# Kernel tuning notes

Measured on AMD Instinct MI355X. Metric: run time of the kernel, lower is better.

## Reference

```python
import jax, jax.numpy as jnp
import numpy as np

NEG_SLOPE = 0.01  # nn.LeakyReLU default used in module

def leaky_relu(x):
    return jnp.where(x >= 0, x, NEG_SLOPE * x)

def setup_inputs() -> dict:
    key = jax.random.key(0)
    k1, k2, k3, k4, k5 = jax.random.split(key, 5)
    B, S, D, H, E = 4, 2048, 1024, 2048, 8
    s_in = 1.0 / np.sqrt(D)
    return {
        "inputs": jax.random.normal(k1, (B, S, D), dtype=jnp.float32),
        "Wg": jax.random.normal(k2, (E, D), dtype=jnp.float32) * s_in,
        "bg": jax.random.normal(k3, (E,), dtype=jnp.float32) * s_in,
        "We": jax.random.normal(k4, (E, H, D), dtype=jnp.float32) * s_in,
        "be": jax.random.normal(k5, (E, H), dtype=jnp.float32) * s_in,
    }

def reference(inputs, Wg, bg, We, be):
    # gate: [B,S,E]
    gate_logits = jnp.einsum('bsd,ed->bse', inputs, Wg) + bg
    gate_probs = jax.nn.softmax(gate_logits, axis=-1)
    # all experts densely: [B,S,E,H]
    expert_out = leaky_relu(jnp.einsum('bsd,ehd->bseh', inputs, We) + be)
    # gate-weighted reduction over experts: [B,S,H]
    weighted = jnp.einsum('bseh,bse->bsh', expert_out, gate_probs)
    return weighted
```

## Files before the change

### kernel.cpp

```cpp
#include <hip/hip_runtime.h>
#include <hip/hip_bf16.h>
#include <math.h>

#define M_TOK 8192
#define N_H   2048
#define K_D   1024
#define N_E   8

typedef __bf16 bf16x8 __attribute__((ext_vector_type(8)));
typedef __bf16 bf16x4 __attribute__((ext_vector_type(4)));
typedef float  f32x4  __attribute__((ext_vector_type(4)));

__device__ inline f32x4 mfma16(bf16x8 a, bf16x8 b, f32x4 c) {
  return __builtin_amdgcn_mfma_f32_16x16x32_bf16(a, b, c, 0, 0, 0);
}

__device__ inline void load16_lds(const void* g, void* l) {
  __builtin_amdgcn_global_load_lds(
      (const __attribute__((address_space(1))) void*)g,
      (__attribute__((address_space(3))) void*)l, 16, 0, 0);
}

__global__ __launch_bounds__(256) void cvt_kernel(const float* __restrict__ src,
                                                  __bf16* __restrict__ dst,
                                                  int n4) {
  int i = blockIdx.x * blockDim.x + threadIdx.x;
  const int stride = gridDim.x * blockDim.x;
  for (; i < n4; i += stride) {
    float4 v = ((const float4*)src)[i];
    bf16x4 o = {(__bf16)v.x, (__bf16)v.y, (__bf16)v.z, (__bf16)v.w};
    *(bf16x4*)(dst + (size_t)i * 4) = o;
  }
}

__global__ __launch_bounds__(256) void gate_kernel(const float* __restrict__ X,
                                                   const float* __restrict__ Wg,
                                                   const float* __restrict__ bg,
                                                   float* __restrict__ gate) {
  const int tid = threadIdx.x;
  const int lane = tid & 63;
  const int wv = tid >> 6;
  const int token = blockIdx.x * 4 + wv;
  const float* xrow = X + (size_t)token * K_D;

  float xr[16];
#pragma unroll
  for (int i = 0; i < 16; ++i) xr[i] = xrow[lane + i * 64];

  float l[N_E];
#pragma unroll
  for (int e = 0; e < N_E; ++e) {
    const float* wrow = Wg + e * K_D;
    float s = 0.f;
#pragma unroll
    for (int i = 0; i < 16; ++i) s += xr[i] * wrow[lane + i * 64];
#pragma unroll
    for (int off = 32; off > 0; off >>= 1) s += __shfl_xor(s, off);
    l[e] = s + bg[e];
  }
  float mx = l[0];
#pragma unroll
  for (int e = 1; e < N_E; ++e) mx = fmaxf(mx, l[e]);
  float p[N_E], den = 0.f;
#pragma unroll
  for (int e = 0; e < N_E; ++e) { p[e] = expf(l[e] - mx); den += p[e]; }
  const float inv = 1.f / den;
  if (lane == 0) {
#pragma unroll
    for (int e = 0; e < N_E; ++e) gate[(size_t)token * N_E + e] = p[e] * inv;
  }
}

__global__ __launch_bounds__(256, 2) void moe_main(
    const __bf16* __restrict__ Xb, const __bf16* __restrict__ Wb,
    const float* __restrict__ gate, const float* __restrict__ be,
    float* __restrict__ out) {
  __shared__ __bf16 As[128 * 32];
  __shared__ __bf16 Bs[256 * 32];
  __shared__ float gS[128 * 8];
  __shared__ float bS[8 * 128];

  const int tid = threadIdx.x;
  const int lane = tid & 63;
  const int wv = tid >> 6;
  const int wr = wv >> 1, wn = wv & 1;
  const int row0 = blockIdx.x * 128;
  const int col0 = blockIdx.y * 128;

  for (int i = tid; i < 1024; i += 256) {
    gS[i] = gate[(size_t)row0 * N_E + i];
    bS[i] = be[(size_t)(i >> 7) * N_H + col0 + (i & 127)];
  }

  const int rA = tid >> 2;
  const int kk = (tid & 3) * 8;
  const __bf16* aP0 = Xb + (size_t)(row0 + rA) * K_D + kk;
  const __bf16* aP1 = aP0 + (size_t)64 * K_D;

  const int lr = lane & 15;
  const int lk = (lane >> 4) * 8;
  const __bf16* aRd = &As[(wr * 64 + lr) * 32 + lk];
  const __bf16* bRd = &Bs[(wn * 64 + lr) * 32 + lk];

  f32x4 fin[4][4];
#pragma unroll
  for (int m = 0; m < 4; ++m)
#pragma unroll
    for (int h = 0; h < 4; ++h) fin[m][h] = (f32x4){0.f, 0.f, 0.f, 0.f};

  for (int p = 0; p < 4; ++p) {
    const int e0 = p * 2;

    const __bf16* bP0 = Wb + ((size_t)(e0 + 0) * N_H + col0 + 0  + rA) * K_D + kk;
    const __bf16* bP1 = Wb + ((size_t)(e0 + 0) * N_H + col0 + 64 + rA) * K_D + kk;
    const __bf16* bP2 = Wb + ((size_t)(e0 + 1) * N_H + col0 + 0  + rA) * K_D + kk;
    const __bf16* bP3 = Wb + ((size_t)(e0 + 1) * N_H + col0 + 64 + rA) * K_D + kk;

    f32x4 acc[4][8];
#pragma unroll
    for (int m = 0; m < 4; ++m)
#pragma unroll
      for (int n = 0; n < 8; ++n) acc[m][n] = (f32x4){0.f, 0.f, 0.f, 0.f};

    for (int kt = 0; kt < K_D / 32; ++kt) {
      const int k0 = kt * 32;
      __syncthreads();
      load16_lds(aP0 + k0, &As[wv * 512]);
      load16_lds(aP1 + k0, &As[2048 + wv * 512]);
      load16_lds(bP0 + k0, &Bs[wv * 512]);
      load16_lds(bP1 + k0, &Bs[2048 + wv * 512]);
      load16_lds(bP2 + k0, &Bs[4096 + wv * 512]);
      load16_lds(bP3 + k0, &Bs[6144 + wv * 512]);
      __syncthreads();

      bf16x8 af[4];
#pragma unroll
      for (int m = 0; m < 4; ++m) af[m] = *(const bf16x8*)(aRd + m * 16 * 32);
#pragma unroll
      for (int n = 0; n < 8; ++n) {
        const bf16x8 bfr =
            *(const bf16x8*)(bRd + ((n >> 2) * 128 + (n & 3) * 16) * 32);
#pragma unroll
        for (int m = 0; m < 4; ++m)
          acc[m][n] = mfma16(af[m], bfr, acc[m][n]);
      }
    }

#pragma unroll
    for (int m = 0; m < 4; ++m) {
#pragma unroll
      for (int j = 0; j < 4; ++j) {
        const int r = wr * 64 + m * 16 + (lane >> 4) * 4 + j;
        const float g0 = gS[r * 8 + e0];
        const float g1 = gS[r * 8 + e0 + 1];
#pragma unroll
        for (int h = 0; h < 4; ++h) {
          const int c = wn * 64 + h * 16 + lr;
          float v0 = acc[m][h][j] + bS[e0 * 128 + c];
          v0 = (v0 >= 0.f) ? v0 : 0.01f * v0;
          float v1 = acc[m][4 + h][j] + bS[(e0 + 1) * 128 + c];
          v1 = (v1 >= 0.f) ? v1 : 0.01f * v1;
          fin[m][h][j] += g0 * v0 + g1 * v1;
        }
      }
    }
  }

#pragma unroll
  for (int m = 0; m < 4; ++m) {
#pragma unroll
    for (int j = 0; j < 4; ++j) {
      const size_t r = (size_t)(row0 + wr * 64 + m * 16 + (lane >> 4) * 4 + j);
#pragma unroll
      for (int h = 0; h < 4; ++h) {
        out[r * N_H + col0 + wn * 64 + h * 16 + lr] = fin[m][h][j];
      }
    }
  }
}

extern "C" void kernel_launch(void* const* d_in, const int* in_sizes, int n_in,
                              void* d_out, int out_size, void* d_ws, size_t ws_size,
                              hipStream_t stream) {
  const float* X  = (const float*)d_in[0];
  const float* Wg = (const float*)d_in[1];
  const float* bg = (const float*)d_in[2];
  const float* We = (const float*)d_in[3];
  const float* be = (const float*)d_in[4];
  float* out = (float*)d_out;

  char* ws = (char*)d_ws;
  __bf16* Xb   = (__bf16*)(ws);
  __bf16* Wb   = (__bf16*)(ws + (size_t)16 * 1024 * 1024);
  float*  gate = (float*)(ws + (size_t)48 * 1024 * 1024);

  cvt_kernel<<<2048, 256, 0, stream>>>(X, Xb, (M_TOK * K_D) / 4);
  cvt_kernel<<<2048, 256, 0, stream>>>(We, Wb, (N_E * N_H * K_D) / 4);

  gate_kernel<<<M_TOK / 4, 256, 0, stream>>>(X, Wg, bg, gate);

  dim3 grid(M_TOK / 128, N_H / 128);
  moe_main<<<grid, 256, 0, stream>>>(Xb, Wb, gate, be, out);
}
```

Measured before the change: 331.9 us.

## Double-buffer LDS in MoE GEMM and fuse X conversion into gate kernel

The main GEMM loop now flattens the four expert-pair passes into one 128-step pipeline. Global-to-LDS loads for the next k-tile go into a second buffer while MFMAs run on the current one, which removes one barrier per step. The gate epilogue is applied every 32 steps, and s_setprio is raised around the MFMA block. The separate fp32-to-bf16 conversion of X is folded into the gate kernel, which already reads X, removing one kernel launch and one full pass over X. LDS use doubles, which may reduce occupancy, and the stores of Xb from the gate kernel are scalar 2-byte writes.

After: 314.2 us. -5.3%, faster.

```diff
diff --git a/kernel.cpp b/kernel.cpp
--- a/kernel.cpp
+++ b/kernel.cpp
@@ -36,7 +36,8 @@
 __global__ __launch_bounds__(256) void gate_kernel(const float* __restrict__ X,
                                                    const float* __restrict__ Wg,
                                                    const float* __restrict__ bg,
-                                                   float* __restrict__ gate) {
+                                                   float* __restrict__ gate,
+                                                   __bf16* __restrict__ Xb) {
   const int tid = threadIdx.x;
   const int lane = tid & 63;
   const int wv = tid >> 6;
@@ -47,6 +48,10 @@
 #pragma unroll
   for (int i = 0; i < 16; ++i) xr[i] = xrow[lane + i * 64];
 
+#pragma unroll
+  for (int i = 0; i < 16; ++i)
+    Xb[(size_t)token * K_D + lane + i * 64] = (__bf16)xr[i];
+
   float l[N_E];
 #pragma unroll
   for (int e = 0; e < N_E; ++e) {
@@ -75,8 +80,8 @@
     const __bf16* __restrict__ Xb, const __bf16* __restrict__ Wb,
     const float* __restrict__ gate, const float* __restrict__ be,
     float* __restrict__ out) {
-  __shared__ __bf16 As[128 * 32];
-  __shared__ __bf16 Bs[256 * 32];
+  __shared__ __bf16 As[2][128 * 32];
+  __shared__ __bf16 Bs[2][256 * 32];
   __shared__ float gS[128 * 8];
   __shared__ float bS[8 * 128];
 
@@ -94,13 +99,15 @@
 
   const int rA = tid >> 2;
   const int kk = (tid & 3) * 8;
-  const __bf16* aP0 = Xb + (size_t)(row0 + rA) * K_D + kk;
-  const __bf16* aP1 = aP0 + (size_t)64 * K_D;
+  const __bf16* aB = Xb + (size_t)(row0 + rA) * K_D + kk;
+  const __bf16* bB = Wb + (size_t)(col0 + rA) * K_D + kk;
 
   const int lr = lane & 15;
   const int lk = (lane >> 4) * 8;
-  const __bf16* aRd = &As[(wr * 64 + lr) * 32 + lk];
-  const __bf16* bRd = &Bs[(wn * 64 + lr) * 32 + lk];
+  const __bf16* aRd0 = &As[0][(wr * 64 + lr) * 32 + lk];
+  const __bf16* aRd1 = &As[1][(wr * 64 + lr) * 32 + lk];
+  const __bf16* bRd0 = &Bs[0][(wn * 64 + lr) * 32 + lk];
+  const __bf16* bRd1 = &Bs[1][(wn * 64 + lr) * 32 + lk];
 
   f32x4 fin[4][4];
 #pragma unroll
@@ -108,44 +115,27 @@
 #pragma unroll
     for (int h = 0; h < 4; ++h) fin[m][h] = (f32x4){0.f, 0.f, 0.f, 0.f};
 
-  for (int p = 0; p < 4; ++p) {
+  f32x4 acc[4][8];
+#pragma unroll
+  for (int m = 0; m < 4; ++m)
+#pragma unroll
+    for (int n = 0; n < 8; ++n) acc[m][n] = (f32x4){0.f, 0.f, 0.f, 0.f};
+
+  auto STAGE = [&](int tn, int bufN) {
+    const int k0 = (tn & 31) << 5;
+    const size_t pOff = (size_t)(tn >> 5) << 22;
+    const __bf16* a = aB + k0;
+    load16_lds(a, &As[bufN][wv * 512]);
+    load16_lds(a + (size_t)64 * K_D, &As[bufN][2048 + wv * 512]);
+    const __bf16* b = bB + pOff + k0;
+    load16_lds(b, &Bs[bufN][wv * 512]);
+    load16_lds(b + (size_t)64 * K_D, &Bs[bufN][2048 + wv * 512]);
+    load16_lds(b + (size_t)N_H * K_D, &Bs[bufN][4096 + wv * 512]);
+    load16_lds(b + (size_t)(N_H + 64) * K_D, &Bs[bufN][6144 + wv * 512]);
+  };
+
+  auto EPI = [&](int p) {
     const int e0 = p * 2;
-
-    const __bf16* bP0 = Wb + ((size_t)(e0 + 0) * N_H + col0 + 0  + rA) * K_D + kk;
-    const __bf16* bP1 = Wb + ((size_t)(e0 + 0) * N_H + col0 + 64 + rA) * K_D + kk;
-    const __bf16* bP2 = Wb + ((size_t)(e0 + 1) * N_H + col0 + 0  + rA) * K_D + kk;
-    const __bf16* bP3 = Wb + ((size_t)(e0 + 1) * N_H + col0 + 64 + rA) * K_D + kk;
-
-    f32x4 acc[4][8];
-#pragma unroll
-    for (int m = 0; m < 4; ++m)
-#pragma unroll
-      for (int n = 0; n < 8; ++n) acc[m][n] = (f32x4){0.f, 0.f, 0.f, 0.f};
-
-    for (int kt = 0; kt < K_D / 32; ++kt) {
-      const int k0 = kt * 32;
-      __syncthreads();
-      load16_lds(aP0 + k0, &As[wv * 512]);
-      load16_lds(aP1 + k0, &As[2048 + wv * 512]);
-      load16_lds(bP0 + k0, &Bs[wv * 512]);
-      load16_lds(bP1 + k0, &Bs[2048 + wv * 512]);
-      load16_lds(bP2 + k0, &Bs[4096 + wv * 512]);
-      load16_lds(bP3 + k0, &Bs[6144 + wv * 512]);
-      __syncthreads();
-
-      bf16x8 af[4];
-#pragma unroll
-      for (int m = 0; m < 4; ++m) af[m] = *(const bf16x8*)(aRd + m * 16 * 32);
-#pragma unroll
-      for (int n = 0; n < 8; ++n) {
-        const bf16x8 bfr =
-            *(const bf16x8*)(bRd + ((n >> 2) * 128 + (n & 3) * 16) * 32);
-#pragma unroll
-        for (int m = 0; m < 4; ++m)
-          acc[m][n] = mfma16(af[m], bfr, acc[m][n]);
-      }
-    }
-
 #pragma unroll
     for (int m = 0; m < 4; ++m) {
 #pragma unroll
@@ -164,6 +154,38 @@
         }
       }
     }
+#pragma unroll
+    for (int m = 0; m < 4; ++m)
+#pragma unroll
+      for (int n = 0; n < 8; ++n) acc[m][n] = (f32x4){0.f, 0.f, 0.f, 0.f};
+  };
+
+  auto STEP = [&](int t, const __bf16* aRd, const __bf16* bRd, int nextBuf) {
+    if (t < 127) STAGE(t + 1, nextBuf);
+    bf16x8 af[4];
+#pragma unroll
+    for (int m = 0; m < 4; ++m) af[m] = *(const bf16x8*)(aRd + m * 512);
+    __builtin_amdgcn_s_setprio(1);
+#pragma unroll
+    for (int n = 0; n < 8; ++n) {
+      const bf16x8 bfr =
+          *(const bf16x8*)(bRd + ((n >> 2) * 128 + (n & 3) * 16) * 32);
+#pragma unroll
+      for (int m = 0; m < 4; ++m)
+        acc[m][n] = mfma16(af[m], bfr, acc[m][n]);
+    }
+    __builtin_amdgcn_s_setprio(0);
+    if ((t & 31) == 31) EPI(t >> 5);
+    __syncthreads();
+  };
+
+  STAGE(0, 0);
+  __syncthreads();
+
+#pragma unroll 1
+  for (int t2 = 0; t2 < 128; t2 += 2) {
+    STEP(t2 + 0, aRd0, bRd0, 1);
+    STEP(t2 + 1, aRd1, bRd1, 0);
   }
 
 #pragma unroll
@@ -194,10 +216,9 @@
   __bf16* Wb   = (__bf16*)(ws + (size_t)16 * 1024 * 1024);
   float*  gate = (float*)(ws + (size_t)48 * 1024 * 1024);
 
-  cvt_kernel<<<2048, 256, 0, stream>>>(X, Xb, (M_TOK * K_D) / 4);
   cvt_kernel<<<2048, 256, 0, stream>>>(We, Wb, (N_E * N_H * K_D) / 4);
 
-  gate_kernel<<<M_TOK / 4, 256, 0, stream>>>(X, Wg, bg, gate);
+  gate_kernel<<<M_TOK / 4, 256, 0, stream>>>(X, Wg, bg, gate, Xb);
 
   dim3 grid(M_TOK / 128, N_H / 128);
   moe_main<<<grid, 256, 0, stream>>>(Xb, Wb, gate, be, out);
```
